# Performance work log

Hardware: AMD Instinct MI355X
Metric: run time of the kernel (lower is better)

## Reference

```python
import jax, jax.numpy as jnp
import numpy as np

ALPHA = 0.2  # LeakyReLU negative slope
N_NODES = 8192
IN_F = 512
OUT_F = 64


def setup_inputs() -> dict:
    key = jax.random.key(0)
    k1, k2, k3, k4, k5 = jax.random.split(key, 5)
    x = jax.random.normal(k1, (N_NODES, IN_F), dtype=jnp.float32)
    n = jax.random.normal(k2, (N_NODES, IN_F), dtype=jnp.float32)
    # nn.Linear default init scale ~ 1/sqrt(fan_in)
    W_tran = jax.random.normal(k3, (OUT_F, IN_F), dtype=jnp.float32) / np.sqrt(IN_F)
    w_att1 = jax.random.normal(k4, (OUT_F,), dtype=jnp.float32) / np.sqrt(OUT_F)
    w_att2 = jax.random.normal(k5, (OUT_F,), dtype=jnp.float32) / np.sqrt(OUT_F)
    return {"x": x, "n": n, "W_tran": W_tran, "w_att1": w_att1, "w_att2": w_att2}


def reference(x, n, W_tran, w_att1, w_att2):
    # h1: [N, out], h2: [N, out]
    h1 = x @ W_tran.T
    h2 = n @ W_tran.T
    # additive attention scores: a[i, j] = att1(h1)_i + att2(h2)_j  -> [N, N]
    s1 = h1 @ w_att1  # [N]
    s2 = h2 @ w_att2  # [N]
    a = s1[:, None] + s2[None, :]
    a = jnp.where(a >= 0, a, ALPHA * a)  # LeakyReLU
    attn = jax.nn.softmax(a, axis=1)     # Softmax(dim=1) over keys
    return attn @ h1  # [N, out]
```

## Files before the change

kernel.cpp:

```cpp
#include <hip/hip_runtime.h>
#include <math.h>

#define NN   8192
#define KF   512
#define DF   64
#define NCH  32
#define NCOL 130

#define BM     64
#define BK     32
#define KSPLIT 4

__global__ void k_prep(const float* __restrict__ W, const float* __restrict__ w2,
                       float* __restrict__ Wt, float* __restrict__ v2) {
    int k = blockIdx.x * 256 + threadIdx.x;
    if (k >= KF) return;
    float a2 = 0.f;
    for (int o = 0; o < DF; ++o) {
        float wv = W[(size_t)o * KF + k];
        Wt[(size_t)k * DF + o] = wv;
        a2 = fmaf(wv, w2[o], a2);
    }
    v2[k] = a2;
}

__global__ __launch_bounds__(256, 2) void k_gemm(const float* __restrict__ x,
        const float* __restrict__ Wt, float* __restrict__ hpart) {
    __shared__ alignas(16) float xs[BK][BM + 4];
    __shared__ alignas(16) float wts[BK][DF];
    const int tid = threadIdx.x;
    const int ty = tid >> 4, tx = tid & 15;
    const int row0 = blockIdx.x * BM;
    const int kbase = blockIdx.y * (KF / KSPLIT);

    float acc[4][4] = {};
    for (int kc = 0; kc < KF / KSPLIT; kc += BK) {
        const int kk = kbase + kc;
        {
            const int r  = tid >> 3;
            const int c4 = (tid & 7) * 4;
            float4 v0 = *reinterpret_cast<const float4*>(x + (size_t)(row0 + r) * KF + kk + c4);
            float4 v1 = *reinterpret_cast<const float4*>(x + (size_t)(row0 + 32 + r) * KF + kk + c4);
            xs[c4 + 0][r] = v0.x; xs[c4 + 1][r] = v0.y; xs[c4 + 2][r] = v0.z; xs[c4 + 3][r] = v0.w;
            xs[c4 + 0][32 + r] = v1.x; xs[c4 + 1][32 + r] = v1.y; xs[c4 + 2][32 + r] = v1.z; xs[c4 + 3][32 + r] = v1.w;
            const float4* src = reinterpret_cast<const float4*>(Wt + (size_t)kk * DF);
            float4* dst = reinterpret_cast<float4*>(&wts[0][0]);
            dst[tid] = src[tid];
            dst[tid + 256] = src[tid + 256];
        }
        __syncthreads();
        #pragma unroll 8
        for (int k = 0; k < BK; ++k) {
            float4 a4 = *reinterpret_cast<const float4*>(&xs[k][ty * 4]);
            float4 b4 = *reinterpret_cast<const float4*>(&wts[k][tx * 4]);
            const float av[4] = {a4.x, a4.y, a4.z, a4.w};
            const float bv[4] = {b4.x, b4.y, b4.z, b4.w};
            #pragma unroll
            for (int i = 0; i < 4; ++i)
                #pragma unroll
                for (int j = 0; j < 4; ++j)
                    acc[i][j] = fmaf(av[i], bv[j], acc[i][j]);
        }
        __syncthreads();
    }
    float* hp = hpart + (size_t)blockIdx.y * NN * DF;
    #pragma unroll
    for (int i = 0; i < 4; ++i)
        *reinterpret_cast<float4*>(hp + (size_t)(row0 + ty * 4 + i) * DF + tx * 4) =
            make_float4(acc[i][0], acc[i][1], acc[i][2], acc[i][3]);
}

__global__ __launch_bounds__(256) void k_combine(const float* __restrict__ hpart,
        const float* __restrict__ w_att1, float* __restrict__ h1, float* __restrict__ s1) {
    const int lane = threadIdx.x & 63, wave = threadIdx.x >> 6;
    const int row = blockIdx.x * 4 + wave;
    float v = 0.f;
    #pragma unroll
    for (int s = 0; s < KSPLIT; ++s) v += hpart[((size_t)s * NN + row) * DF + lane];
    h1[(size_t)row * DF + lane] = v;
    float p = v * w_att1[lane];
    #pragma unroll
    for (int off = 32; off; off >>= 1) p += __shfl_xor(p, off);
    if (lane == 0) s1[row] = p;
}

__global__ __launch_bounds__(256) void k_s2(const float* __restrict__ n,
        const float* __restrict__ v2, float* __restrict__ s2) {
    const int lane = threadIdx.x & 63;
    const int row = (blockIdx.x * 256 + threadIdx.x) >> 6;
    const float4* a = reinterpret_cast<const float4*>(n + (size_t)row * KF);
    const float4* b = reinterpret_cast<const float4*>(v2);
    float acc = 0.f;
    #pragma unroll
    for (int c = 0; c < 2; ++c) {
        float4 av = a[lane + c * 64], bv = b[lane + c * 64];
        acc = fmaf(av.x, bv.x, fmaf(av.y, bv.y, fmaf(av.z, bv.z, fmaf(av.w, bv.w, acc))));
    }
    #pragma unroll
    for (int off = 32; off; off >>= 1) acc += __shfl_xor(acc, off);
    if (lane == 0) s2[row] = acc;
}

__global__ __launch_bounds__(256) void k_count(const float* __restrict__ s2,
                                               int* __restrict__ partial) {
    __shared__ float sk[256];
    const int j = blockIdx.x * 256 + threadIdx.x;
    const int k0 = blockIdx.y * 256;
    sk[threadIdx.x] = s2[k0 + threadIdx.x];
    __syncthreads();
    const float mine = s2[j];
    int cnt = 0;
    #pragma unroll 8
    for (int t = 0; t < 256; ++t) {
        float v = sk[t];
        int idx = k0 + t;
        cnt += (v < mine) || (v == mine && idx < j);
    }
    partial[(size_t)blockIdx.y * NN + j] = cnt;
}

__global__ __launch_bounds__(256) void k_scatter(const float* __restrict__ s2,
        const int* __restrict__ partial, int* __restrict__ order,
        float* __restrict__ s2s, double* __restrict__ wpos, double* __restrict__ wneg) {
    const int j = blockIdx.x * 256 + threadIdx.x;
    int r = 0;
    for (int kb = 0; kb < NCH; ++kb) r += partial[(size_t)kb * NN + j];
    const float v = s2[j];
    order[r] = j;
    s2s[r] = v;
    wpos[r] = exp((double)v);
    wneg[r] = exp(0.2 * (double)v);
}

__global__ __launch_bounds__(256) void k_chunksum(const float* __restrict__ h1,
        const int* __restrict__ order, const double* __restrict__ wpos,
        const double* __restrict__ wneg, double* __restrict__ cT) {
    __shared__ double red[256];
    const int col = blockIdx.x >> 5, c = blockIdx.x & 31;
    const int p = c * 256 + threadIdx.x;
    const double wgt = (col < 65) ? wpos[p] : wneg[p];
    const int d = (col < 65) ? col : col - 65;
    double val = (d < DF) ? wgt * (double)h1[(size_t)order[p] * DF + d] : wgt;
    red[threadIdx.x] = val;
    __syncthreads();
    for (int s = 128; s; s >>= 1) {
        if (threadIdx.x < s) red[threadIdx.x] += red[threadIdx.x + s];
        __syncthreads();
    }
    if (threadIdx.x == 0) cT[blockIdx.x] = red[0];
}

__global__ void k_chunkscan(const double* __restrict__ cT, double* __restrict__ cO,
                            double* __restrict__ E) {
    const int col = threadIdx.x;
    if (col >= NCOL) return;
    double run = 0.0;
    for (int c = 0; c < NCH; ++c) {
        cO[(size_t)col * NCH + c] = run;
        run += cT[(size_t)col * NCH + c];
    }
    E[(size_t)NN * NCOL + col] = run;
}

__global__ __launch_bounds__(256) void k_scan(const float* __restrict__ h1,
        const int* __restrict__ order, const double* __restrict__ wpos,
        const double* __restrict__ wneg, const double* __restrict__ cO,
        double* __restrict__ E) {
    __shared__ double buf[2][256];
    const int col = blockIdx.x >> 5, c = blockIdx.x & 31;
    const int tid = threadIdx.x;
    const int p = c * 256 + tid;
    const double wgt = (col < 65) ? wpos[p] : wneg[p];
    const int d = (col < 65) ? col : col - 65;
    double val = (d < DF) ? wgt * (double)h1[(size_t)order[p] * DF + d] : wgt;
    buf[0][tid] = val;
    int cur = 0;
    for (int off = 1; off < 256; off <<= 1) {
        __syncthreads();
        double t = buf[cur][tid];
        if (tid >= off) t += buf[cur][tid - off];
        buf[cur ^ 1][tid] = t;
        cur ^= 1;
    }
    __syncthreads();
    const double excl = tid ? buf[cur][tid - 1] : 0.0;
    E[(size_t)p * NCOL + col] = cO[blockIdx.x] + excl;
}

__global__ __launch_bounds__(256) void k_out(const float* __restrict__ s1,
        const float* __restrict__ s2s, const double* __restrict__ E,
        float* __restrict__ out) {
    const int lane = threadIdx.x & 63, wave = threadIdx.x >> 6;
    const int i = blockIdx.x * 4 + wave;
    const float s1v = s1[i];
    const float t = -s1v;
    int lo = 0, hi = NN;
    while (lo < hi) {
        int mid = (lo + hi) >> 1;
        if (s2s[mid] < t) lo = mid + 1; else hi = mid;
    }
    const double* Ek = E + (size_t)lo * NCOL;
    const double* Et = E + (size_t)NN * NCOL;
    const double e1 = exp((double)s1v);
    const double e2 = exp(0.2 * (double)s1v);
    const double num = e1 * (Et[lane] - Ek[lane]) + e2 * Ek[65 + lane];
    const double den = e1 * (Et[DF] - Ek[DF]) + e2 * Ek[65 + DF];
    out[(size_t)i * DF + lane] = (float)(num / den);
}

extern "C" void kernel_launch(void* const* d_in, const int* in_sizes, int n_in,
                              void* d_out, int out_size, void* d_ws, size_t ws_size,
                              hipStream_t stream) {
    const float* x  = (const float*)d_in[0];
    const float* nmat = (const float*)d_in[1];
    const float* W  = (const float*)d_in[2];
    const float* w1 = (const float*)d_in[3];
    const float* w2 = (const float*)d_in[4];
    float* out = (float*)d_out;

    char* ws = (char*)d_ws;
    size_t off = 0;
    auto alloc = [&](size_t bytes) -> void* {
        void* p = ws + off;
        off += (bytes + 255) & ~(size_t)255;
        return p;
    };
    float*  Wt      = (float*)alloc((size_t)KF * DF * 4);
    float*  v2      = (float*)alloc((size_t)KF * 4);
    float*  h1      = (float*)alloc((size_t)NN * DF * 4);
    float*  s1      = (float*)alloc((size_t)NN * 4);
    float*  s2      = (float*)alloc((size_t)NN * 4);
    int*    partial = (int*)alloc((size_t)NCH * NN * 4);
    int*    order   = (int*)alloc((size_t)NN * 4);
    float*  s2s     = (float*)alloc((size_t)NN * 4);
    double* wpos    = (double*)alloc((size_t)NN * 8);
    double* wneg    = (double*)alloc((size_t)NN * 8);
    double* cT      = (double*)alloc((size_t)NCOL * NCH * 8);
    double* cO      = (double*)alloc((size_t)NCOL * NCH * 8);
    double* E       = (double*)alloc((size_t)(NN + 1) * NCOL * 8);
    float*  hpart   = (float*)E;

    k_prep<<<2, 256, 0, stream>>>(W, w2, Wt, v2);
    k_gemm<<<dim3(NN / BM, KSPLIT), 256, 0, stream>>>(x, Wt, hpart);
    k_combine<<<NN / 4, 256, 0, stream>>>(hpart, w1, h1, s1);
    k_s2<<<NN / 4, 256, 0, stream>>>(nmat, v2, s2);
    k_count<<<dim3(NCH, NCH), 256, 0, stream>>>(s2, partial);
    k_scatter<<<NCH, 256, 0, stream>>>(s2, partial, order, s2s, wpos, wneg);
    k_chunksum<<<NCOL * NCH, 256, 0, stream>>>(h1, order, wpos, wneg, cT);
    k_chunkscan<<<1, 256, 0, stream>>>(cT, cO, E);
    k_scan<<<NCOL * NCH, 256, 0, stream>>>(h1, order, wpos, wneg, cO, E);
    k_out<<<NN / 4, 256, 0, stream>>>(s1, s2s, E, out);
}
```

Before: 76.60 us.

## Compute x@W^T with split-bf16 MFMA (three-product hi/lo emulation of fp32)

The fp32 SIMT tiled GEMM for h1 is replaced by MFMA bf16 16x16x32 instructions. x and W are each split into high and low bf16 parts, and three products (hh, lh, hl) are accumulated to approximate fp32 accuracy. Each block converts its 64x128 slice of x into LDS once, and W fragments are read straight from global memory. This aims to cut the GEMM's arithmetic cost by using matrix cores, at some risk of small precision loss and uncoalesced scalar output stores.

```diff
diff --git a/kernel.cpp b/kernel.cpp
--- a/kernel.cpp
+++ b/kernel.cpp
@@ -1,73 +1,88 @@
 #include <hip/hip_runtime.h>
 #include <math.h>
 
-#define NN   8192
-#define KF   512
-#define DF   64
-#define NCH  32
-#define NCOL 130
-
-#define BM     64
-#define BK     32
+#define NN    8192
+#define KF    512
+#define DF    64
+#define NCH   32
+#define NCOL  130
 #define KSPLIT 4
 
-__global__ void k_prep(const float* __restrict__ W, const float* __restrict__ w2,
-                       float* __restrict__ Wt, float* __restrict__ v2) {
-    int k = blockIdx.x * 256 + threadIdx.x;
-    if (k >= KF) return;
+typedef __attribute__((ext_vector_type(8))) short bf16x8;
+typedef __attribute__((ext_vector_type(4))) float f32x4;
+
+__device__ __forceinline__ unsigned short f2bf_rn(float f) {
+    unsigned u = __float_as_uint(f);
+    unsigned r = (u + 0x7fffu + ((u >> 16) & 1u)) >> 16;
+    return (unsigned short)r;
+}
+__device__ __forceinline__ float bf2f(unsigned short s) {
+    return __uint_as_float(((unsigned)s) << 16);
+}
+
+__global__ __launch_bounds__(256) void k_prep(const float* __restrict__ W,
+        const float* __restrict__ w2, float* __restrict__ v2,
+        unsigned short* __restrict__ Wh, unsigned short* __restrict__ Wl) {
+    const int k = blockIdx.x * 256 + threadIdx.x;
     float a2 = 0.f;
     for (int o = 0; o < DF; ++o) {
-        float wv = W[(size_t)o * KF + k];
-        Wt[(size_t)k * DF + o] = wv;
+        const float wv = W[(size_t)o * KF + k];
         a2 = fmaf(wv, w2[o], a2);
+        const unsigned short hi = f2bf_rn(wv);
+        Wh[(size_t)o * KF + k] = hi;
+        Wl[(size_t)o * KF + k] = f2bf_rn(wv - bf2f(hi));
     }
     v2[k] = a2;
 }
 
-__global__ __launch_bounds__(256, 2) void k_gemm(const float* __restrict__ x,
-        const float* __restrict__ Wt, float* __restrict__ hpart) {
-    __shared__ alignas(16) float xs[BK][BM + 4];
-    __shared__ alignas(16) float wts[BK][DF];
+__global__ __launch_bounds__(256) void k_gemm(const float* __restrict__ x,
+        const unsigned short* __restrict__ Wh, const unsigned short* __restrict__ Wl,
+        float* __restrict__ hpart) {
+    __shared__ unsigned short xh[64][136];
+    __shared__ unsigned short xl[64][136];
     const int tid = threadIdx.x;
-    const int ty = tid >> 4, tx = tid & 15;
-    const int row0 = blockIdx.x * BM;
-    const int kbase = blockIdx.y * (KF / KSPLIT);
-
-    float acc[4][4] = {};
-    for (int kc = 0; kc < KF / KSPLIT; kc += BK) {
-        const int kk = kbase + kc;
-        {
-            const int r  = tid >> 3;
-            const int c4 = (tid & 7) * 4;
-            float4 v0 = *reinterpret_cast<const float4*>(x + (size_t)(row0 + r) * KF + kk + c4);
-            float4 v1 = *reinterpret_cast<const float4*>(x + (size_t)(row0 + 32 + r) * KF + kk + c4);
-            xs[c4 + 0][r] = v0.x; xs[c4 + 1][r] = v0.y; xs[c4 + 2][r] = v0.z; xs[c4 + 3][r] = v0.w;
-            xs[c4 + 0][32 + r] = v1.x; xs[c4 + 1][32 + r] = v1.y; xs[c4 + 2][32 + r] = v1.z; xs[c4 + 3][32 + r] = v1.w;
-            const float4* src = reinterpret_cast<const float4*>(Wt + (size_t)kk * DF);
-            float4* dst = reinterpret_cast<float4*>(&wts[0][0]);
-            dst[tid] = src[tid];
-            dst[tid + 256] = src[tid + 256];
+    const int rb = blockIdx.x & 127, ks = blockIdx.x >> 7;
+    const int row0 = rb * 64, kbase = ks * (KF / KSPLIT);
+    {
+        const int r = tid >> 2, q = tid & 3;
+        const float* xr = x + (size_t)(row0 + r) * KF + kbase + q * 32;
+        #pragma unroll
+        for (int i = 0; i < 8; ++i) {
+            const float4 v = *reinterpret_cast<const float4*>(xr + i * 4);
+            ushort4 h, l;
+            h.x = f2bf_rn(v.x); l.x = f2bf_rn(v.x - bf2f(h.x));
+            h.y = f2bf_rn(v.y); l.y = f2bf_rn(v.y - bf2f(h.y));
+            h.z = f2bf_rn(v.z); l.z = f2bf_rn(v.z - bf2f(h.z));
+            h.w = f2bf_rn(v.w); l.w = f2bf_rn(v.w - bf2f(h.w));
+            *reinterpret_cast<ushort4*>(&xh[r][q * 32 + i * 4]) = h;
+            *reinterpret_cast<ushort4*>(&xl[r][q * 32 + i * 4]) = l;
         }
-        __syncthreads();
-        #pragma unroll 8
-        for (int k = 0; k < BK; ++k) {
-            float4 a4 = *reinterpret_cast<const float4*>(&xs[k][ty * 4]);
-            float4 b4 = *reinterpret_cast<const float4*>(&wts[k][tx * 4]);
-            const float av[4] = {a4.x, a4.y, a4.z, a4.w};
-            const float bv[4] = {b4.x, b4.y, b4.z, b4.w};
-            #pragma unroll
-            for (int i = 0; i < 4; ++i)
-                #pragma unroll
-                for (int j = 0; j < 4; ++j)
-                    acc[i][j] = fmaf(av[i], bv[j], acc[i][j]);
+    }
+    __syncthreads();
+    const int w = tid >> 6, l = tid & 63;
+    const int fr = l & 15, fq = l >> 4;
+    f32x4 acc[4] = {{0.f,0.f,0.f,0.f},{0.f,0.f,0.f,0.f},{0.f,0.f,0.f,0.f},{0.f,0.f,0.f,0.f}};
+    #pragma unroll
+    for (int kstep = 0; kstep < 4; ++kstep) {
+        const int k0 = kstep * 32;
+        const bf16x8 ah = *reinterpret_cast<const bf16x8*>(&xh[w * 16 + fr][k0 + fq * 8]);
+        const bf16x8 al = *reinterpret_cast<const bf16x8*>(&xl[w * 16 + fr][k0 + fq * 8]);
+        #pragma unroll
+        for (int cg = 0; cg < 4; ++cg) {
+            const size_t wb = (size_t)(cg * 16 + fr) * KF + kbase + k0 + fq * 8;
+            const bf16x8 bh = *reinterpret_cast<const bf16x8*>(Wh + wb);
+            const bf16x8 bl = *reinterpret_cast<const bf16x8*>(Wl + wb);
+            acc[cg] = __builtin_amdgcn_mfma_f32_16x16x32_bf16(ah, bh, acc[cg], 0, 0, 0);
+            acc[cg] = __builtin_amdgcn_mfma_f32_16x16x32_bf16(al, bh, acc[cg], 0, 0, 0);
+            acc[cg] = __builtin_amdgcn_mfma_f32_16x16x32_bf16(ah, bl, acc[cg], 0, 0, 0);
         }
-        __syncthreads();
-    }
-    float* hp = hpart + (size_t)blockIdx.y * NN * DF;
-    #pragma unroll
-    for (int i = 0; i < 4; ++i)
-        *reinterpret_cast<float4*>(hp + (size_t)(row0 + ty * 4 + i) * DF + tx * 4) =
-            make_float4(acc[i][0], acc[i][1], acc[i][2], acc[i][3]);
+    }
+    float* hp = hpart + (size_t)ks * NN * DF;
+    #pragma unroll
+    for (int cg = 0; cg < 4; ++cg)
+        #pragma unroll
+        for (int j = 0; j < 4; ++j)
+            hp[(size_t)(row0 + w * 16 + fq * 4 + j) * DF + cg * 16 + fr] = acc[cg][j];
 }
 
 __global__ __launch_bounds__(256) void k_combine(const float* __restrict__ hpart,
@@ -211,11 +226,11 @@
 extern "C" void kernel_launch(void* const* d_in, const int* in_sizes, int n_in,
                               void* d_out, int out_size, void* d_ws, size_t ws_size,
                               hipStream_t stream) {
-    const float* x  = (const float*)d_in[0];
+    const float* x    = (const float*)d_in[0];
     const float* nmat = (const float*)d_in[1];
-    const float* W  = (const float*)d_in[2];
-    const float* w1 = (const float*)d_in[3];
-    const float* w2 = (const float*)d_in[4];
+    const float* W    = (const float*)d_in[2];
+    const float* w1   = (const float*)d_in[3];
+    const float* w2   = (const float*)d_in[4];
     float* out = (float*)d_out;
 
     char* ws = (char*)d_ws;
@@ -225,7 +240,8 @@
         off += (bytes + 255) & ~(size_t)255;
         return p;
     };
-    float*  Wt      = (float*)alloc((size_t)KF * DF * 4);
+    unsigned short* Wh = (unsigned short*)alloc((size_t)DF * KF * 2);
+    unsigned short* Wl = (unsigned short*)alloc((size_t)DF * KF * 2);
     float*  v2      = (float*)alloc((size_t)KF * 4);
     float*  h1      = (float*)alloc((size_t)NN * DF * 4);
     float*  s1      = (float*)alloc((size_t)NN * 4);
@@ -240,8 +256,8 @@
     double* E       = (double*)alloc((size_t)(NN + 1) * NCOL * 8);
     float*  hpart   = (float*)E;
 
-    k_prep<<<2, 256, 0, stream>>>(W, w2, Wt, v2);
-    k_gemm<<<dim3(NN / BM, KSPLIT), 256, 0, stream>>>(x, Wt, hpart);
+    k_prep<<<2, 256, 0, stream>>>(W, w2, v2, Wh, Wl);
+    k_gemm<<<512, 256, 0, stream>>>(x, Wh, Wl, hpart);
     k_combine<<<NN / 4, 256, 0, stream>>>(hpart, w1, h1, s1);
     k_s2<<<NN / 4, 256, 0, stream>>>(nmat, v2, s2);
     k_count<<<dim3(NCH, NCH), 256, 0, stream>>>(s2, partial);
```

After: 78.75 us. 1.03x slower.
